# Performance work log

Measured on AMD Instinct MI355X. Metric: run time of the kernel, lower is better.

## Reference

```python
import jax, jax.numpy as jnp
import numpy as np

IN_FEATURES = 1024
OUT_FEATURES = 1024


def setup_inputs() -> dict:
    key = jax.random.key(0)
    k_x, k_w, k_b = jax.random.split(key, 3)
    # input activations [batch, seq, in_features]
    x = jax.random.normal(k_x, (4, 8192, IN_FEATURES), dtype=jnp.float32)
    # kaiming_uniform_(a=sqrt(5)) on [out, in] -> bound = 1/sqrt(in_features)
    bound = 1.0 / np.sqrt(IN_FEATURES)
    weight = jax.random.uniform(k_w, (OUT_FEATURES, IN_FEATURES), dtype=jnp.float32,
                                minval=-bound, maxval=bound)
    bias = jax.random.uniform(k_b, (OUT_FEATURES,), dtype=jnp.float32,
                              minval=-bound, maxval=bound)
    # adiabatic binarization scale factors (non-trainable scalars)
    kk = jnp.float32(10.0)
    aa = jnp.float32(1.0)
    return {"x": x, "weight": weight, "bias": bias, "kk": kk, "aa": aa}


def reference(x, weight, bias, kk, aa):
    # BinaryLinearFunction: soft-binarize the weight with learned scales, then GEMM.
    # w_bin = aa * clamp(kk * w, -1, 1)  (annealed binarization; kk -> inf gives sign(w))
    w_bin = aa * jnp.clip(kk * weight, -1.0, 1.0)  # [out, in]
    # out[b, s, o] = sum_i x[b, s, i] * w_bin[o, i] + bias[o]
    return jnp.einsum('bsi,oi->bso', x, w_bin) + bias
```

## Files before the change

### kernel.cpp

```cpp
#include <hip/hip_runtime.h>
#include <stdint.h>

#define K_DIM 1024
#define N_DIM 1024
#define BM 128
#define BN 256
#define BK 32
#define NT (K_DIM / BK)
#define AOFF_U32 (BM * 16)
#define UNIT_U32 ((BM + BN) * 16)
#define NRING 3

#define AS1 __attribute__((address_space(1)))
#define AS3 __attribute__((address_space(3)))

typedef __attribute__((ext_vector_type(4))) float f32x4;
typedef __attribute__((ext_vector_type(8))) short bf16x8;
typedef __attribute__((ext_vector_type(4))) uint32_t u32x4;

__device__ __forceinline__ uint32_t pack_bf16(float a, float b) {
  uint32_t ua = __builtin_bit_cast(uint32_t, a) + 0x8000u;
  uint32_t ub = __builtin_bit_cast(uint32_t, b) + 0x8000u;
  return __builtin_amdgcn_perm(ub, ua, 0x07060302u);
}

__device__ __forceinline__ float wbin1(float v, float kkv, float aav) {
  float t = v * kkv;
  t = fminf(fmaxf(t, -1.0f), 1.0f);
  return t * aav;
}

__global__ __launch_bounds__(256) void wconv(const float* __restrict__ w,
                                             const float* __restrict__ kkp,
                                             const float* __restrict__ aap,
                                             uint32_t* __restrict__ wb) {
  const float kkv = kkp[0];
  const float aav = aap[0];
  const int g = blockIdx.x * 256 + threadIdx.x;
  const f32x4* src = (const f32x4*)(w + (size_t)g * 16);
  f32x4 v0 = src[0], v1 = src[1], v2 = src[2], v3 = src[3];
  uint32_t p[8];
#pragma unroll
  for (int i = 0; i < 4; ++i) {
    f32x4 v = i == 0 ? v0 : (i == 1 ? v1 : (i == 2 ? v2 : v3));
    p[2 * i] = pack_bf16(wbin1(v[0], kkv, aav), wbin1(v[1], kkv, aav));
    p[2 * i + 1] = pack_bf16(wbin1(v[2], kkv, aav), wbin1(v[3], kkv, aav));
  }
  u32x4* dst = (u32x4*)(wb + (size_t)g * 8);
  dst[0] = u32x4{p[0], p[1], p[2], p[3]};
  dst[1] = u32x4{p[4], p[5], p[6], p[7]};
}

__global__ __launch_bounds__(512, 4) void binlin_fused(
    const float* __restrict__ x, const uint32_t* __restrict__ wb,
    const float* __restrict__ bias, float* __restrict__ out) {
  __shared__ uint32_t lds[NRING * UNIT_U32];

  const int tid = threadIdx.x;

  const int per = gridDim.x >> 3;
  const int logical = (blockIdx.x & 7) * per + (blockIdx.x >> 3);
  const int mIdx = logical >> 2;
  const int nIdx = logical & 3;
  const int row0 = mIdx * BM;
  const int col0 = nIdx * BN;

  const int w8 = tid >> 6;
  const int lane = tid & 63;

  const int arow = w8 * 16 + (lane >> 2);
  const int aslot = lane & 3;
  const float* ga = x + (size_t)(row0 + arow) * K_DIM + aslot * 8;
  const int awidx = arow * 16 + ((aslot ^ ((arow >> 1) & 3)) * 4);

  const int rl = lane >> 2;
  const int sl = (lane & 3) ^ ((lane >> 3) & 3);
  const uint32_t* gb_base =
      wb + (size_t)(col0 + w8 * 32 + rl) * (K_DIM / 2) + sl * 4;

  const int wr = w8 >> 2;
  const int wc = w8 & 3;
  const int cl = lane & 15;
  const int kg = lane >> 4;

  f32x4 acc[4][4] = {};
  bf16x8 af[4], bfr[2];
  f32x4 aA, aB;

#define STAGE_B1(kt, SD, c)                                               \
  __builtin_amdgcn_global_load_lds(                                       \
      (const AS1 uint32_t*)(gb_base + (size_t)((c)*16) * (K_DIM / 2) +    \
                            (kt)*16),                                     \
      (AS3 uint32_t*)((SD) + AOFF_U32 + (w8 * 32 + (c)*16) * 16), 16, 0, 0)

#define LOAD_A(kt)                                        \
  do {                                                    \
    aA = *(const f32x4*)(ga + (kt)*32);                   \
    aB = *(const f32x4*)(ga + (kt)*32 + 4);               \
  } while (0)

#define PACK_WRITE_A(SD)                                                  \
  do {                                                                    \
    u32x4 pk = {pack_bf16(aA[0], aA[1]), pack_bf16(aA[2], aA[3]),         \
                pack_bf16(aB[0], aB[1]), pack_bf16(aB[2], aB[3])};        \
    *(u32x4*)((SD) + awidx) = pk;                                         \
  } while (0)

#define READ_AF(AB)                                                            \
  _Pragma("unroll") for (int m = 0; m < 4; ++m) {                              \
    int rr = wr * 64 + m * 16 + cl;                                            \
    af[m] =                                                                    \
        *(const bf16x8*)((AB) + rr * 16 + ((kg ^ ((rr >> 1) & 3)) * 4));       \
  }

#define READ_BF(BB, NH)                                                        \
  _Pragma("unroll") for (int n = 0; n < 2; ++n) {                              \
    int rr = wc * 64 + ((NH)*2 + n) * 16 + cl;                                 \
    bfr[n] =                                                                   \
        *(const bf16x8*)((BB) + rr * 16 + ((kg ^ ((rr >> 1) & 3)) * 4));       \
  }

#define MFMA_CL(NH)                                                            \
  __builtin_amdgcn_s_setprio(1);                                               \
  _Pragma("unroll") for (int m = 0; m < 4; ++m)                                \
  _Pragma("unroll") for (int n = 0; n < 2; ++n)                                \
  acc[m][(NH)*2 + n] = __builtin_amdgcn_mfma_f32_16x16x32_bf16(                \
      af[m], bfr[n], acc[m][(NH)*2 + n], 0, 0, 0);                             \
  __builtin_amdgcn_s_setprio(0);

  f32x4 p0a = *(const f32x4*)(ga + 0);
  f32x4 p0b = *(const f32x4*)(ga + 4);
  f32x4 p1a = *(const f32x4*)(ga + 32);
  f32x4 p1b = *(const f32x4*)(ga + 36);
  STAGE_B1(0, &lds[0], 0);
  STAGE_B1(0, &lds[0], 1);
  STAGE_B1(1, &lds[UNIT_U32], 0);
  STAGE_B1(1, &lds[UNIT_U32], 1);
  {
    u32x4 pk0 = {pack_bf16(p0a[0], p0a[1]), pack_bf16(p0a[2], p0a[3]),
                 pack_bf16(p0b[0], p0b[1]), pack_bf16(p0b[2], p0b[3])};
    *(u32x4*)(&lds[0] + awidx) = pk0;
    u32x4 pk1 = {pack_bf16(p1a[0], p1a[1]), pack_bf16(p1a[2], p1a[3]),
                 pack_bf16(p1b[0], p1b[1]), pack_bf16(p1b[2], p1b[3])};
    *(u32x4*)(&lds[UNIT_U32] + awidx) = pk1;
  }
  asm volatile("s_waitcnt vmcnt(2)" ::: "memory");
  asm volatile("s_waitcnt lgkmcnt(0)" ::: "memory");
  __builtin_amdgcn_s_barrier();

  int cu = 0, su = 2;
  for (int t = 0; t < NT; ++t) {
    const uint32_t* AB = &lds[cu * UNIT_U32];
    const uint32_t* BB = AB + AOFF_U32;
    uint32_t* SD = &lds[su * UNIT_U32];
    const bool more = (t + 2) < NT;
    if (more) {
      LOAD_A(t + 2);
      STAGE_B1(t + 2, SD, 0);
      STAGE_B1(t + 2, SD, 1);
    }
    READ_AF(AB);
    READ_BF(BB, 0);
    MFMA_CL(0);
    READ_BF(BB, 1);
    MFMA_CL(1);
    if (more) {
      asm volatile("s_waitcnt vmcnt(2)" ::: "memory");
      PACK_WRITE_A(SD);
      asm volatile("s_waitcnt lgkmcnt(0)" ::: "memory");
      __builtin_amdgcn_s_barrier();
    } else if (t == NT - 2) {
      asm volatile("s_waitcnt vmcnt(0)" ::: "memory");
      __builtin_amdgcn_s_barrier();
    }
    cu = (cu == NRING - 1) ? 0 : cu + 1;
    su = (su == NRING - 1) ? 0 : su + 1;
  }

#pragma unroll
  for (int n = 0; n < 4; ++n) {
    int col = col0 + wc * 64 + n * 16 + cl;
    float bv = bias[col];
#pragma unroll
    for (int m = 0; m < 4; ++m) {
      int rowb = row0 + wr * 64 + m * 16 + kg * 4;
#pragma unroll
      for (int i = 0; i < 4; ++i) {
        out[(size_t)(rowb + i) * N_DIM + col] = acc[m][n][i] + bv;
      }
    }
  }
#undef STAGE_B1
#undef LOAD_A
#undef PACK_WRITE_A
#undef READ_AF
#undef READ_BF
#undef MFMA_CL
}

extern "C" void kernel_launch(void* const* d_in, const int* in_sizes, int n_in,
                              void* d_out, int out_size, void* d_ws, size_t ws_size,
                              hipStream_t stream) {
  const float* x = (const float*)d_in[0];
  const float* w = (const float*)d_in[1];
  const float* bias = (const float*)d_in[2];
  const float* kk = (const float*)d_in[3];
  const float* aa = (const float*)d_in[4];
  float* out = (float*)d_out;

  uint32_t* wb = (uint32_t*)d_ws;
  wconv<<<(N_DIM * K_DIM) / (256 * 16), 256, 0, stream>>>(w, kk, aa, wb);

  const int M = in_sizes[0] / K_DIM;
  const int grid = (M / BM) * (N_DIM / BN);
  binlin_fused<<<grid, 512, 0, stream>>>(x, wb, bias, out);
}
```

Baseline: 112.9 us.

## Enlarge GEMM tile to 256x256 with four-stage LDS ring and deeper prefetch

Doubles the M tile from 128 to 256 rows so each block computes a 256x256 output tile with 8x4 MFMA accumulators per wave, halving redundant B-tile loads per output. The LDS ring grows from three to four stages, with loads issued three tiles ahead, and the loop is unrolled by two with ping-ponged register sets for the fp32 A prefetch. The A conversion is spread across all threads (two halves per row). This costs more registers (occupancy hint drops to 2 blocks) and more LDS, and it halves the grid size, which may reduce latency hiding.

Measured after the change: 143.4 us. 26.9% more time.

```diff
diff --git a/kernel.cpp b/kernel.cpp
--- a/kernel.cpp
+++ b/kernel.cpp
@@ -3,13 +3,12 @@
 
 #define K_DIM 1024
 #define N_DIM 1024
-#define BM 128
+#define BM 256
 #define BN 256
 #define BK 32
 #define NT (K_DIM / BK)
 #define AOFF_U32 (BM * 16)
 #define UNIT_U32 ((BM + BN) * 16)
-#define NRING 3
 
 #define AS1 __attribute__((address_space(1)))
 #define AS3 __attribute__((address_space(3)))
@@ -51,10 +50,10 @@
   dst[1] = u32x4{p[4], p[5], p[6], p[7]};
 }
 
-__global__ __launch_bounds__(512, 4) void binlin_fused(
+__global__ __launch_bounds__(512, 2) void binlin_fused4(
     const float* __restrict__ x, const uint32_t* __restrict__ wb,
     const float* __restrict__ bias, float* __restrict__ out) {
-  __shared__ uint32_t lds[NRING * UNIT_U32];
+  __shared__ uint32_t lds[4 * UNIT_U32];
 
   const int tid = threadIdx.x;
 
@@ -68,10 +67,12 @@
   const int w8 = tid >> 6;
   const int lane = tid & 63;
 
-  const int arow = w8 * 16 + (lane >> 2);
-  const int aslot = lane & 3;
-  const float* ga = x + (size_t)(row0 + arow) * K_DIM + aslot * 8;
-  const int awidx = arow * 16 + ((aslot ^ ((arow >> 1) & 3)) * 4);
+  const int r = tid >> 1;
+  const int h = tid & 1;
+  const float* ga = x + (size_t)(row0 + r) * K_DIM + h * 16;
+  const int sw = (r >> 1) & 3;
+  const int awidx0 = r * 16 + (((h * 2) ^ sw) * 4);
+  const int awidx1 = r * 16 + (((h * 2 + 1) ^ sw) * 4);
 
   const int rl = lane >> 2;
   const int sl = (lane & 3) ^ ((lane >> 3) & 3);
@@ -83,98 +84,107 @@
   const int cl = lane & 15;
   const int kg = lane >> 4;
 
-  f32x4 acc[4][4] = {};
-  bf16x8 af[4], bfr[2];
-  f32x4 aA, aB;
-
-#define STAGE_B1(kt, SD, c)                                               \
-  __builtin_amdgcn_global_load_lds(                                       \
-      (const AS1 uint32_t*)(gb_base + (size_t)((c)*16) * (K_DIM / 2) +    \
-                            (kt)*16),                                     \
+  f32x4 acc[8][4] = {};
+  bf16x8 af[8], bfr[2][2];
+  f32x4 XA0, XA1, XA2, XA3, XB0, XB1, XB2, XB3;
+
+#define LOAD_A4(kt, R0, R1, R2, R3)                            \
+  do {                                                         \
+    const f32x4* pa = (const f32x4*)(ga + (size_t)(kt) * 32);  \
+    R0 = pa[0]; R1 = pa[1]; R2 = pa[2]; R3 = pa[3];            \
+  } while (0)
+
+#define PACK_A(SD, R0, R1, R2, R3)                                       \
+  do {                                                                   \
+    u32x4 q0 = {pack_bf16(R0[0], R0[1]), pack_bf16(R0[2], R0[3]),        \
+                pack_bf16(R1[0], R1[1]), pack_bf16(R1[2], R1[3])};       \
+    u32x4 q1 = {pack_bf16(R2[0], R2[1]), pack_bf16(R2[2], R2[3]),        \
+                pack_bf16(R3[0], R3[1]), pack_bf16(R3[2], R3[3])};       \
+    *(u32x4*)((SD) + awidx0) = q0;                                       \
+    *(u32x4*)((SD) + awidx1) = q1;                                       \
+  } while (0)
+
+#define STAGE_B1(kt, SD, c)                                              \
+  __builtin_amdgcn_global_load_lds(                                      \
+      (const AS1 uint32_t*)(gb_base + (size_t)((c)*16) * (K_DIM / 2) +   \
+                            (kt)*16),                                    \
       (AS3 uint32_t*)((SD) + AOFF_U32 + (w8 * 32 + (c)*16) * 16), 16, 0, 0)
 
-#define LOAD_A(kt)                                        \
-  do {                                                    \
-    aA = *(const f32x4*)(ga + (kt)*32);                   \
-    aB = *(const f32x4*)(ga + (kt)*32 + 4);               \
+#define READ_AF(AB)                                                          \
+  _Pragma("unroll") for (int m = 0; m < 8; ++m) {                            \
+    int rr = wr * 128 + m * 16 + cl;                                         \
+    af[m] =                                                                  \
+        *(const bf16x8*)((AB) + rr * 16 + ((kg ^ ((rr >> 1) & 3)) * 4));     \
+  }
+
+#define READ_BF(BB, NH)                                                      \
+  _Pragma("unroll") for (int n = 0; n < 2; ++n) {                            \
+    int rr = wc * 64 + ((NH)*2 + n) * 16 + cl;                               \
+    bfr[NH][n] =                                                             \
+        *(const bf16x8*)((BB) + rr * 16 + ((kg ^ ((rr >> 1) & 3)) * 4));     \
+  }
+
+#define MFMA_CL(NH)                                                          \
+  __builtin_amdgcn_s_setprio(1);                                             \
+  _Pragma("unroll") for (int m = 0; m < 8; ++m)                              \
+  _Pragma("unroll") for (int n = 0; n < 2; ++n)                              \
+  acc[m][(NH)*2 + n] = __builtin_amdgcn_mfma_f32_16x16x32_bf16(              \
+      af[m], bfr[NH][n], acc[m][(NH)*2 + n], 0, 0, 0);                       \
+  __builtin_amdgcn_s_setprio(0);
+
+#define TILE(T, PA0, PA1, PA2, PA3, PL0, PL1, PL2, PL3)                      \
+  do {                                                                       \
+    const int t_ = (T);                                                      \
+    const uint32_t* AB = &lds[(t_ & 3) * UNIT_U32];                          \
+    const uint32_t* BB = AB + AOFF_U32;                                      \
+    uint32_t* SD3 = &lds[((t_ + 3) & 3) * UNIT_U32];                         \
+    uint32_t* SD2 = &lds[((t_ + 2) & 3) * UNIT_U32];                         \
+    const bool more3 = (t_ + 3) < NT;                                        \
+    const bool more2 = (t_ + 2) < NT;                                        \
+    if (more3) {                                                             \
+      LOAD_A4(t_ + 3, PL0, PL1, PL2, PL3);                                   \
+      STAGE_B1(t_ + 3, SD3, 0);                                              \
+      STAGE_B1(t_ + 3, SD3, 1);                                              \
+    }                                                                        \
+    READ_AF(AB);                                                             \
+    READ_BF(BB, 0);                                                          \
+    MFMA_CL(0);                                                              \
+    if (more2) {                                                             \
+      if (more3) {                                                           \
+        asm volatile("s_waitcnt vmcnt(8)" ::: "memory");                     \
+      } else {                                                               \
+        asm volatile("s_waitcnt vmcnt(2)" ::: "memory");                     \
+      }                                                                      \
+      PACK_A(SD2, PA0, PA1, PA2, PA3);                                       \
+    }                                                                        \
+    READ_BF(BB, 1);                                                          \
+    MFMA_CL(1);                                                              \
+    if (t_ == NT - 2) asm volatile("s_waitcnt vmcnt(0)" ::: "memory");       \
+    if (t_ < NT - 1) {                                                       \
+      asm volatile("s_waitcnt lgkmcnt(0)" ::: "memory");                     \
+      __builtin_amdgcn_s_barrier();                                          \
+    }                                                                        \
   } while (0)
 
-#define PACK_WRITE_A(SD)                                                  \
-  do {                                                                    \
-    u32x4 pk = {pack_bf16(aA[0], aA[1]), pack_bf16(aA[2], aA[3]),         \
-                pack_bf16(aB[0], aB[1]), pack_bf16(aB[2], aB[3])};        \
-    *(u32x4*)((SD) + awidx) = pk;                                         \
-  } while (0)
-
-#define READ_AF(AB)                                                            \
-  _Pragma("unroll") for (int m = 0; m < 4; ++m) {                              \
-    int rr = wr * 64 + m * 16 + cl;                                            \
-    af[m] =                                                                    \
-        *(const bf16x8*)((AB) + rr * 16 + ((kg ^ ((rr >> 1) & 3)) * 4));       \
-  }
-
-#define READ_BF(BB, NH)                                                        \
-  _Pragma("unroll") for (int n = 0; n < 2; ++n) {                              \
-    int rr = wc * 64 + ((NH)*2 + n) * 16 + cl;                                 \
-    bfr[n] =                                                                   \
-        *(const bf16x8*)((BB) + rr * 16 + ((kg ^ ((rr >> 1) & 3)) * 4));       \
-  }
-
-#define MFMA_CL(NH)                                                            \
-  __builtin_amdgcn_s_setprio(1);                                               \
-  _Pragma("unroll") for (int m = 0; m < 4; ++m)                                \
-  _Pragma("unroll") for (int n = 0; n < 2; ++n)                                \
-  acc[m][(NH)*2 + n] = __builtin_amdgcn_mfma_f32_16x16x32_bf16(                \
-      af[m], bfr[n], acc[m][(NH)*2 + n], 0, 0, 0);                             \
-  __builtin_amdgcn_s_setprio(0);
-
-  f32x4 p0a = *(const f32x4*)(ga + 0);
-  f32x4 p0b = *(const f32x4*)(ga + 4);
-  f32x4 p1a = *(const f32x4*)(ga + 32);
-  f32x4 p1b = *(const f32x4*)(ga + 36);
+  f32x4 A00, A01, A02, A03, A10, A11, A12, A13;
+  LOAD_A4(0, A00, A01, A02, A03);
   STAGE_B1(0, &lds[0], 0);
   STAGE_B1(0, &lds[0], 1);
+  LOAD_A4(1, A10, A11, A12, A13);
   STAGE_B1(1, &lds[UNIT_U32], 0);
   STAGE_B1(1, &lds[UNIT_U32], 1);
-  {
-    u32x4 pk0 = {pack_bf16(p0a[0], p0a[1]), pack_bf16(p0a[2], p0a[3]),
-                 pack_bf16(p0b[0], p0b[1]), pack_bf16(p0b[2], p0b[3])};
-    *(u32x4*)(&lds[0] + awidx) = pk0;
-    u32x4 pk1 = {pack_bf16(p1a[0], p1a[1]), pack_bf16(p1a[2], p1a[3]),
-                 pack_bf16(p1b[0], p1b[1]), pack_bf16(p1b[2], p1b[3])};
-    *(u32x4*)(&lds[UNIT_U32] + awidx) = pk1;
-  }
-  asm volatile("s_waitcnt vmcnt(2)" ::: "memory");
+  LOAD_A4(2, XA0, XA1, XA2, XA3);
+  STAGE_B1(2, &lds[2 * UNIT_U32], 0);
+  STAGE_B1(2, &lds[2 * UNIT_U32], 1);
+  PACK_A(&lds[0], A00, A01, A02, A03);
+  PACK_A(&lds[UNIT_U32], A10, A11, A12, A13);
+  asm volatile("s_waitcnt vmcnt(6)" ::: "memory");
   asm volatile("s_waitcnt lgkmcnt(0)" ::: "memory");
   __builtin_amdgcn_s_barrier();
 
-  int cu = 0, su = 2;
-  for (int t = 0; t < NT; ++t) {
-    const uint32_t* AB = &lds[cu * UNIT_U32];
-    const uint32_t* BB = AB + AOFF_U32;
-    uint32_t* SD = &lds[su * UNIT_U32];
-    const bool more = (t + 2) < NT;
-    if (more) {
-      LOAD_A(t + 2);
-      STAGE_B1(t + 2, SD, 0);
-      STAGE_B1(t + 2, SD, 1);
-    }
-    READ_AF(AB);
-    READ_BF(BB, 0);
-    MFMA_CL(0);
-    READ_BF(BB, 1);
-    MFMA_CL(1);
-    if (more) {
-      asm volatile("s_waitcnt vmcnt(2)" ::: "memory");
-      PACK_WRITE_A(SD);
-      asm volatile("s_waitcnt lgkmcnt(0)" ::: "memory");
-      __builtin_amdgcn_s_barrier();
-    } else if (t == NT - 2) {
-      asm volatile("s_waitcnt vmcnt(0)" ::: "memory");
-      __builtin_amdgcn_s_barrier();
-    }
-    cu = (cu == NRING - 1) ? 0 : cu + 1;
-    su = (su == NRING - 1) ? 0 : su + 1;
+  for (int t2 = 0; t2 < NT; t2 += 2) {
+    TILE(t2, XA0, XA1, XA2, XA3, XB0, XB1, XB2, XB3);
+    TILE(t2 + 1, XB0, XB1, XB2, XB3, XA0, XA1, XA2, XA3);
   }
 
 #pragma unroll
@@ -182,20 +192,21 @@
     int col = col0 + wc * 64 + n * 16 + cl;
     float bv = bias[col];
 #pragma unroll
-    for (int m = 0; m < 4; ++m) {
-      int rowb = row0 + wr * 64 + m * 16 + kg * 4;
+    for (int m = 0; m < 8; ++m) {
+      int rowb = row0 + wr * 128 + m * 16 + kg * 4;
 #pragma unroll
       for (int i = 0; i < 4; ++i) {
         out[(size_t)(rowb + i) * N_DIM + col] = acc[m][n][i] + bv;
       }
     }
   }
+#undef LOAD_A4
+#undef PACK_A
 #undef STAGE_B1
-#undef LOAD_A
-#undef PACK_WRITE_A
 #undef READ_AF
 #undef READ_BF
 #undef MFMA_CL
+#undef TILE
 }
 
 extern "C" void kernel_launch(void* const* d_in, const int* in_sizes, int n_in,
@@ -213,5 +224,5 @@
 
   const int M = in_sizes[0] / K_DIM;
   const int grid = (M / BM) * (N_DIM / BN);
-  binlin_fused<<<grid, 512, 0, stream>>>(x, wb, bias, out);
-}
+  binlin_fused4<<<grid, 512, 0, stream>>>(x, wb, bias, out);
+}
```
